# Kernel optimization log

Hardware: AMD Instinct MI355X
Metric: run time of the kernel (lower is better)

The kernel has to match this reference:

```python
import jax, jax.numpy as jnp
import numpy as np

H = 1024      # hidden_dim == memory_dim (required by seq-axis concat)
M = 1024      # memory_dim
FF = 4096     # ff_dim
WIN = 16      # window_size
SLOTS = 10    # persistent memory slots
B, S = 2, 4096
EPS_LN = 1e-5
EPS_NORM = 1e-12


def _layernorm(x, g, b):
    m = jnp.mean(x, axis=-1, keepdims=True)
    v = jnp.var(x, axis=-1, keepdims=True)
    return (x - m) / jnp.sqrt(v + EPS_LN) * g + b


def setup_inputs() -> dict:
    key = jax.random.key(0)
    ks = jax.random.split(key, 12)

    def lin_w(k, out_d, in_d):
        return jax.random.normal(k, (out_d, in_d), jnp.float32) / np.sqrt(in_d)

    return {
        "x": jax.random.normal(ks[0], (B, S, H), jnp.float32),
        "mem_W": lin_w(ks[1], M, M), "mem_b": jnp.zeros((M,), jnp.float32),
        "P": jax.random.normal(ks[2], (SLOTS, M), jnp.float32),
        "Wi": lin_w(ks[3], M, H), "bi": jnp.zeros((M,), jnp.float32),
        "Wl1": lin_w(ks[4], M, M), "bl1": jnp.zeros((M,), jnp.float32),
        "Wl2": lin_w(ks[5], M, M), "bl2": jnp.zeros((M,), jnp.float32),
        "Wo": lin_w(ks[6], H, M), "bo": jnp.zeros((H,), jnp.float32),
        "fgate": jnp.ones((1,), jnp.float32),
        "lrate": jnp.ones((1,), jnp.float32),
        "Wg": lin_w(ks[7], H, 2 * H), "bg": jnp.zeros((H,), jnp.float32),
        "W1": lin_w(ks[8], FF, H), "b1": jnp.zeros((FF,), jnp.float32),
        "W2": lin_w(ks[9], H, FF), "b2": jnp.zeros((H,), jnp.float32),
        "g1": jnp.ones((H,), jnp.float32), "be1": jnp.zeros((H,), jnp.float32),
        "g2": jnp.ones((H,), jnp.float32), "be2": jnp.zeros((H,), jnp.float32),
        "g3": jnp.ones((H,), jnp.float32), "be3": jnp.zeros((H,), jnp.float32),
    }


def reference(x, mem_W, mem_b, P, Wi, bi, Wl1, bl1, Wl2, bl2, Wo, bo,
              fgate, lrate, Wg, bg, W1, b1, W2, b2,
              g1, be1, g2, be2, g3, be3):
    b, s, h = x.shape
    # k = concat(x, persistent) along seq; v = k.clone()
    k_full = jnp.concatenate([x, jnp.broadcast_to(P, (b,) + P.shape)], axis=1)  # [B, S+SLOTS, H]

    # sit at positions >= S and are never inside the window, so only x is attended.
    idx = jnp.arange(s)[:, None] + jnp.arange(-WIN, 1)[None, :]
    valid = idx >= 0
    k_win = k_full[:, jnp.maximum(idx, 0)]
    scores = jnp.einsum('bsh,bswh->bsw', x, k_win) * (h ** -0.5)
    scores = jnp.where(valid[None], scores, -jnp.inf)
    attn_out = jnp.einsum('bsw,bswh->bsh', jax.nn.softmax(scores, axis=-1), k_win)
    x1 = _layernorm(x + attn_out, g1, be1)

    # --- neural long-term memory (key == value since v = k.clone())
    kv = k_full.reshape(-1, h)
    kn = kv / jnp.maximum(jnp.linalg.norm(kv, axis=-1, keepdims=True), EPS_NORM)
    kp = kn @ Wi.T + bi          # projected key; value_proj is identical
    vp = kp
    hdd = jax.nn.silu(kp @ Wl1.T + bl1)
    hdd = jax.nn.silu(hdd @ Wl2.T + bl2)
    pred = hdd @ mem_W.T + mem_b
    diff = pred - vp
    n, m = diff.shape
    grad_W = (2.0 / (n * m)) * diff.T @ hdd          # d mse / d mem_W
    W_new = (1.0 - fgate) * mem_W + lrate * grad_W   # test-time memory update
    mem_out = hdd @ W_new.T + mem_b
    mo = (mem_out @ Wo.T + bo).reshape(b, -1, h)[:, :s]  # align with x seq length

    # --- gated fusion + FFN
    gate = jax.nn.sigmoid(jnp.concatenate([x1, mo], axis=-1) @ Wg.T + bg)
    combined = gate * x1 + (1.0 - gate) * mo
    x2 = _layernorm(x1 + combined, g2, be2)
    ff = jax.nn.silu(x2 @ W1.T + b1) @ W2.T + b2
    return _layernorm(x2 + ff, g3, be3)
```

## Files before the change

kernel.cpp:

```cpp
#include <hip/hip_runtime.h>
#include <hip/hip_bf16.h>

#define WIN 16
#define SLOTS 10
#define SS 4096
#define NTOK 8192
#define NKV 8212
#define NPOS 4106

typedef unsigned short u16;
typedef unsigned int u32;
typedef __attribute__((ext_vector_type(8))) short short8;
typedef __attribute__((ext_vector_type(4))) float f32x4;

__device__ __forceinline__ u16 f2bf(float f){
  union { float f; u32 u; } a; a.f = f;
  u32 r = (a.u + 0x7fff + ((a.u >> 16) & 1)) >> 16;
  return (u16)r;
}
__device__ __forceinline__ float bf2f(u16 v){
  union { u32 u; float f; } a; a.u = ((u32)v) << 16;
  return a.f;
}

#define GLOAD(gp, lp) __builtin_amdgcn_global_load_lds( \
    (const __attribute__((address_space(1))) void*)(gp), \
    (__attribute__((address_space(3))) void*)(lp), 16, 0, 0)

#define FENCE_BARRIER() do { \
    __builtin_amdgcn_sched_barrier(0); \
    __builtin_amdgcn_s_barrier(); \
    __builtin_amdgcn_sched_barrier(0); \
  } while(0)

__global__ __launch_bounds__(256) void cvt_bf16(const float4* __restrict__ in,
                                                ushort4* __restrict__ out, int n4){
  int i = blockIdx.x * 256 + threadIdx.x;
  if (i < n4){
    float4 v = in[i];
    ushort4 o; o.x=f2bf(v.x); o.y=f2bf(v.y); o.z=f2bf(v.z); o.w=f2bf(v.w);
    out[i] = o;
  }
}

__global__ __launch_bounds__(256) void attn_ln1(
    const float* __restrict__ x, const float* __restrict__ g1,
    const float* __restrict__ be1, u16* __restrict__ x1b)
{
  const int n = blockIdx.x;
  const int b = n >> 12, s = n & 4095;
  const int t = threadIdx.x, lane = t & 63, w = t >> 6;
  const float* xb = x + ((size_t)b << 22);
  const float4 q = ((const float4*)(xb + ((size_t)s << 10)))[t];
  const int j0 = (s >= WIN) ? 0 : (WIN - s);
  float kvv[17][4];
  float part[17];
  #pragma unroll
  for (int j=0;j<17;j++){
    float4 kk = make_float4(0.f,0.f,0.f,0.f);
    if (j >= j0) kk = ((const float4*)(xb + ((size_t)(s - WIN + j) << 10)))[t];
    kvv[j][0]=kk.x; kvv[j][1]=kk.y; kvv[j][2]=kk.z; kvv[j][3]=kk.w;
    part[j] = q.x*kk.x + q.y*kk.y + q.z*kk.z + q.w*kk.w;
  }
  __shared__ float red[17][4];
  #pragma unroll
  for (int j=0;j<17;j++){
    float v = part[j];
    #pragma unroll
    for (int off=32; off; off>>=1) v += __shfl_xor(v, off, 64);
    if (lane == 0) red[j][w] = v;
  }
  __syncthreads();
  __shared__ float wsh[17];
  if (t == 0){
    float sc[17];
    float mx = -3.0e38f;
    #pragma unroll
    for (int j=0;j<17;j++){
      float v = (red[j][0]+red[j][1]+red[j][2]+red[j][3]) * 0.03125f;
      sc[j] = v;
      if (j >= j0) mx = fmaxf(mx, v);
    }
    float ssum = 0.f;
    #pragma unroll
    for (int j=0;j<17;j++){
      float e = (j >= j0) ? expf(sc[j]-mx) : 0.f;
      wsh[j] = e; ssum += e;
    }
    float inv = 1.f/ssum;
    #pragma unroll
    for (int j=0;j<17;j++) wsh[j] *= inv;
  }
  __syncthreads();
  float y0=q.x, y1=q.y, y2=q.z, y3=q.w;
  #pragma unroll
  for (int j=0;j<17;j++){
    float wj = wsh[j];
    y0 += wj*kvv[j][0]; y1 += wj*kvv[j][1]; y2 += wj*kvv[j][2]; y3 += wj*kvv[j][3];
  }
  float s1 = y0+y1+y2+y3;
  float s2 = y0*y0+y1*y1+y2*y2+y3*y3;
  #pragma unroll
  for (int off=32; off; off>>=1){ s1 += __shfl_xor(s1, off, 64); s2 += __shfl_xor(s2, off, 64); }
  __shared__ float rsh[8];
  if (lane == 0){ rsh[w] = s1; rsh[4+w] = s2; }
  __syncthreads();
  float S1 = rsh[0]+rsh[1]+rsh[2]+rsh[3];
  float S2 = rsh[4]+rsh[5]+rsh[6]+rsh[7];
  float mean = S1 * (1.f/1024.f);
  float var  = S2 * (1.f/1024.f) - mean*mean;
  float rstd = 1.f/sqrtf(var + 1e-5f);
  float4 gv = ((const float4*)g1)[t];
  float4 bv = ((const float4*)be1)[t];
  ushort4 ob;
  ob.x = f2bf((y0-mean)*rstd*gv.x + bv.x);
  ob.y = f2bf((y1-mean)*rstd*gv.y + bv.y);
  ob.z = f2bf((y2-mean)*rstd*gv.z + bv.z);
  ob.w = f2bf((y3-mean)*rstd*gv.w + bv.w);
  ((ushort4*)x1b)[((size_t)n << 8) + t] = ob;
}

__global__ __launch_bounds__(256) void kv_norm(const float* __restrict__ x,
                                               const float* __restrict__ P,
                                               u16* __restrict__ kn)
{
  const int r = blockIdx.x;
  const int t = threadIdx.x, lane = t & 63, w = t >> 6;
  const int b = r / NPOS;
  const int pos = r - b*NPOS;
  const float* src = (pos < SS) ? (x + (((size_t)b*SS + pos) << 10))
                                : (P + ((size_t)(pos - SS) << 10));
  float4 v = ((const float4*)src)[t];
  float s2 = v.x*v.x + v.y*v.y + v.z*v.z + v.w*v.w;
  #pragma unroll
  for (int off=32; off; off>>=1) s2 += __shfl_xor(s2, off, 64);
  __shared__ float sh[4];
  if (lane == 0) sh[w] = s2;
  __syncthreads();
  float S = sh[0]+sh[1]+sh[2]+sh[3];
  float inv = 1.f / fmaxf(sqrtf(S), 1e-12f);
  ushort4 o; o.x=f2bf(v.x*inv); o.y=f2bf(v.y*inv); o.z=f2bf(v.z*inv); o.w=f2bf(v.w*inv);
  ((ushort4*)kn)[((size_t)r << 8) + t] = o;
}

template<int EPI, int SPLITA>
__global__ __launch_bounds__(256) void gemm_nt(
    const u16* __restrict__ A, const u16* __restrict__ A2,
    const u16* __restrict__ Bmat, const float* __restrict__ bias,
    const u16* __restrict__ auxb,
    float* __restrict__ Cf, u16* __restrict__ Cb,
    int N, int O, int ldA, int ldB, int klen)
{
  __shared__ __align__(16) u16 lA[2][128*64];
  __shared__ __align__(16) u16 lB[2][128*64];
  const int t = threadIdx.x;
  const int lane = t & 63;
  const int bm0 = blockIdx.x * 128;
  const int bn0 = blockIdx.y * 128;
  const int wid = t >> 6;
  const int wr = wid >> 1, wc = wid & 1;
  const int nkt = klen >> 6;

  f32x4 acc[4][4];
  #pragma unroll
  for (int i=0;i<4;i++)
    #pragma unroll
    for (int j=0;j<4;j++)
      acc[i][j] = (f32x4){0.f,0.f,0.f,0.f};

  const int srow = t >> 3;
  const int schunk = (((t & 7) ^ ((t >> 3) & 7)) << 3);

  auto stage = [&](int kt, int buf){
    const int kbase = kt << 6;
    #pragma unroll
    for (int i=0;i<4;i++){
      int gr = bm0 + srow + i*32; gr = gr < N ? gr : N-1;
      const u16* src;
      if (SPLITA){
        src = (kbase < 1024) ? (A  + (size_t)gr*(size_t)ldA + kbase + schunk)
                             : (A2 + ((size_t)gr << 10) + (kbase - 1024) + schunk);
      } else {
        src = A + (size_t)gr*(size_t)ldA + kbase + schunk;
      }
      GLOAD(src, &lA[buf][(i*256 + t) << 3]);
    }
    #pragma unroll
    for (int i=0;i<4;i++){
      int gr = bn0 + srow + i*32; gr = gr < O ? gr : O-1;
      const u16* src = Bmat + (size_t)gr*(size_t)ldB + kbase + schunk;
      GLOAD(src, &lB[buf][(i*256 + t) << 3]);
    }
  };

  stage(0, 0);
  if (nkt > 1) stage(1, 1);

  const int l15 = lane & 15;
  const int rx = l15 & 7;
  const int cq = lane >> 4;

  for (int kt = 0; kt < nkt; ++kt){
    const int cur = kt & 1;
    if (kt + 1 < nkt) { asm volatile("s_waitcnt vmcnt(8)" ::: "memory"); }
    else              { asm volatile("s_waitcnt vmcnt(0)" ::: "memory"); }
    FENCE_BARRIER();
    #pragma unroll
    for (int kk=0;kk<2;kk++){
      const int soff = (((kk*4 + cq) ^ rx) << 3);
      short8 af[4], bfv[4];
      #pragma unroll
      for (int mi=0;mi<4;mi++)
        af[mi] = *(const short8*)(&lA[cur][((wr*64 + mi*16 + l15) << 6) + soff]);
      #pragma unroll
      for (int ni=0;ni<4;ni++)
        bfv[ni] = *(const short8*)(&lB[cur][((wc*64 + ni*16 + l15) << 6) + soff]);
      #pragma unroll
      for (int mi=0;mi<4;mi++)
        #pragma unroll
        for (int ni=0;ni<4;ni++)
          acc[mi][ni] = __builtin_amdgcn_mfma_f32_16x16x32_bf16(af[mi], bfv[ni], acc[mi][ni], 0, 0, 0);
    }
    FENCE_BARRIER();
    if (kt + 2 < nkt) stage(kt + 2, cur);
  }

  const int rbase = (lane >> 4) * 4;
  const int cidx = lane & 15;
  #pragma unroll
  for (int mi=0;mi<4;mi++){
    #pragma unroll
    for (int r=0;r<4;r++){
      const int n = bm0 + wr*64 + mi*16 + rbase + r;
      if (n >= N) continue;
      #pragma unroll
      for (int ni=0;ni<4;ni++){
        const int o = bn0 + wc*64 + ni*16 + cidx;
        float v = acc[mi][ni][r] + bias[o];
        if (EPI == 6){
          int b = n / NPOS;
          int pos = n - b*NPOS;
          if (pos < SS){
            Cb[(((size_t)(b*SS + pos)) << 10) + o] = f2bf(v);
          }
        } else {
          size_t idx = (size_t)n*(size_t)O + o;
          if (EPI == 0){ Cf[idx] = v; }
          else if (EPI == 1){ float sv = v/(1.f+__expf(-v)); Cb[idx] = f2bf(sv); }
          else if (EPI == 2){ Cb[idx] = f2bf(v); }
          else if (EPI == 4){ Cb[idx] = f2bf(v - bf2f(auxb[idx])); }
          else if (EPI == 5){ Cb[idx] = f2bf(1.f/(1.f+__expf(-v))); }
        }
      }
    }
  }
}

#define NSPLIT 6
__global__ __launch_bounds__(256) void gemm_tn(
    const u16* __restrict__ A, const u16* __restrict__ B,
    float* __restrict__ part0, float* __restrict__ part1)
{
  __shared__ __align__(16) u16 lA[128*64];
  __shared__ __align__(16) u16 lB[128*64];
  const int t = threadIdx.x, lane = t & 63;
  const int i0 = blockIdx.x * 128, j0 = blockIdx.y * 128, z = blockIdx.z;
  const int wid = t >> 6, wr = wid >> 1, wc = wid & 1;
  const int TILES = (NKV + 63) >> 6;
  const int PER = (TILES + NSPLIT - 1) / NSPLIT;
  const int kt0 = z * PER;
  const int ktend = (kt0 + PER < TILES) ? (kt0 + PER) : TILES;

  f32x4 acc[4][4];
  #pragma unroll
  for (int i=0;i<4;i++)
    #pragma unroll
    for (int j=0;j<4;j++)
      acc[i][j] = (f32x4){0.f,0.f,0.f,0.f};

  const int p = t & 31;
  const int g = t >> 5;

  auto loadr = [&](int kt, short8 R[8]){
    const int n0 = kt << 6;
    const int na = n0 + 2*p, nb = na + 1;
    short8 z8 = (short8){0,0,0,0,0,0,0,0};
    R[0]=z8;R[1]=z8;R[2]=z8;R[3]=z8;R[4]=z8;R[5]=z8;R[6]=z8;R[7]=z8;
    if (na < NKV){
      const u16* ra = A + (size_t)na*1024 + i0 + g*16;
      R[0] = *(const short8*)ra; R[1] = *(const short8*)(ra+8);
      const u16* rb = B + (size_t)na*1024 + j0 + g*16;
      R[4] = *(const short8*)rb; R[5] = *(const short8*)(rb+8);
    }
    if (nb < NKV){
      const u16* ra = A + (size_t)nb*1024 + i0 + g*16;
      R[2] = *(const short8*)ra; R[3] = *(const short8*)(ra+8);
      const u16* rb = B + (size_t)nb*1024 + j0 + g*16;
      R[6] = *(const short8*)rb; R[7] = *(const short8*)(rb+8);
    }
  };

  short8 cr[8], nr[8];
  loadr(kt0, cr);

  const int pc = p >> 2, pl = p & 3;

  for (int kt = kt0; kt < ktend; ++kt){
    if (kt + 1 < ktend) loadr(kt + 1, nr);
    asm volatile("" ::: "memory");
    FENCE_BARRIER();
    u32* wA = (u32*)lA; u32* wB = (u32*)lB;
    #pragma unroll
    for (int e=0;e<8;e++){
      const int s = (pc ^ e) * 4 + pl;
      wA[(g*16 + e)*32 + s]     = ((u32)(u16)cr[0][e]) | (((u32)(u16)cr[2][e]) << 16);
      wB[(g*16 + e)*32 + s]     = ((u32)(u16)cr[4][e]) | (((u32)(u16)cr[6][e]) << 16);
    }
    #pragma unroll
    for (int e=0;e<8;e++){
      const int s = (pc ^ e) * 4 + pl;
      wA[(g*16 + 8 + e)*32 + s] = ((u32)(u16)cr[1][e]) | (((u32)(u16)cr[3][e]) << 16);
      wB[(g*16 + 8 + e)*32 + s] = ((u32)(u16)cr[5][e]) | (((u32)(u16)cr[7][e]) << 16);
    }
    asm volatile("s_waitcnt lgkmcnt(0)" ::: "memory");
    FENCE_BARRIER();
    const int l15 = lane & 15;
    const int rx = l15 & 7;
    const int cq = lane >> 4;
    #pragma unroll
    for (int kk=0;kk<2;kk++){
      const int soff = (((kk*4 + cq) ^ rx) << 3);
      short8 af[4], bfv[4];
      #pragma unroll
      for (int mi=0;mi<4;mi++)
        af[mi] = *(const short8*)(lA + ((wr*64 + mi*16 + l15) << 6) + soff);
      #pragma unroll
      for (int ni=0;ni<4;ni++)
        bfv[ni] = *(const short8*)(lB + ((wc*64 + ni*16 + l15) << 6) + soff);
      #pragma unroll
      for (int mi=0;mi<4;mi++)
        #pragma unroll
        for (int ni=0;ni<4;ni++)
          acc[mi][ni] = __builtin_amdgcn_mfma_f32_16x16x32_bf16(af[mi], bfv[ni], acc[mi][ni], 0, 0, 0);
    }
    #pragma unroll
    for (int e=0;e<8;e++) cr[e] = nr[e];
  }

  float* dst = (z < 4) ? (part0 + ((size_t)z << 20)) : (part1 + ((size_t)(z-4) << 20));
  const int rbase = (lane >> 4) * 4;
  const int cidx = lane & 15;
  #pragma unroll
  for (int mi=0;mi<4;mi++)
    #pragma unroll
    for (int r=0;r<4;r++){
      const int i = i0 + wr*64 + mi*16 + rbase + r;
      #pragma unroll
      for (int ni=0;ni<4;ni++){
        const int j = j0 + wc*64 + ni*16 + cidx;
        dst[((size_t)i << 10) + j] = acc[mi][ni][r];
      }
    }
}

__global__ __launch_bounds__(256) void wnew_k(const float* __restrict__ part0,
                                              const float* __restrict__ part1,
                                              const float* __restrict__ memW,
                                              const float* __restrict__ fg,
                                              const float* __restrict__ lr,
                                              u16* __restrict__ out)
{
  int i = blockIdx.x*256 + threadIdx.x;
  float s = part0[i] + part0[i + (1<<20)] + part0[i + (2<<20)] + part0[i + (3<<20)]
          + part1[i] + part1[i + (1<<20)];
  const float scale = 2.f / ((float)NKV * 1024.f);
  float v = (1.f - fg[0])*memW[i] + lr[0]*scale*s;
  out[i] = f2bf(v);
}

__global__ __launch_bounds__(256) void ln_gate(
    const u16* __restrict__ x1b, const u16* __restrict__ gateb,
    const u16* __restrict__ mob, const float* __restrict__ g2,
    const float* __restrict__ be2, u16* __restrict__ x2b)
{
  const int n = blockIdx.x;
  const int t = threadIdx.x, lane = t & 63, w = t >> 6;
  const size_t rb = (size_t)n << 8;
  ushort4 xa = ((const ushort4*)x1b)[rb+t];
  ushort4 ga = ((const ushort4*)gateb)[rb+t];
  ushort4 ma = ((const ushort4*)mob)[rb+t];
  float a0=bf2f(xa.x),a1=bf2f(xa.y),a2=bf2f(xa.z),a3=bf2f(xa.w);
  float g0=bf2f(ga.x),g1v=bf2f(ga.y),g2v=bf2f(ga.z),g3v=bf2f(ga.w);
  float m0=bf2f(ma.x),m1=bf2f(ma.y),m2=bf2f(ma.z),m3=bf2f(ma.w);
  float y0 = a0 + g0*a0 + (1.f-g0)*m0;
  float y1 = a1 + g1v*a1 + (1.f-g1v)*m1;
  float y2 = a2 + g2v*a2 + (1.f-g2v)*m2;
  float y3 = a3 + g3v*a3 + (1.f-g3v)*m3;
  float s1 = y0+y1+y2+y3;
  float s2 = y0*y0+y1*y1+y2*y2+y3*y3;
  #pragma unroll
  for (int off=32; off; off>>=1){ s1 += __shfl_xor(s1, off, 64); s2 += __shfl_xor(s2, off, 64); }
  __shared__ float rsh[8];
  if (lane == 0){ rsh[w] = s1; rsh[4+w] = s2; }
  __syncthreads();
  float S1 = rsh[0]+rsh[1]+rsh[2]+rsh[3];
  float S2 = rsh[4]+rsh[5]+rsh[6]+rsh[7];
  float mean = S1 * (1.f/1024.f);
  float var  = S2 * (1.f/1024.f) - mean*mean;
  float rstd = 1.f/sqrtf(var + 1e-5f);
  float4 gv = ((const float4*)g2)[t];
  float4 bv = ((const float4*)be2)[t];
  ushort4 ob;
  ob.x = f2bf((y0-mean)*rstd*gv.x + bv.x);
  ob.y = f2bf((y1-mean)*rstd*gv.y + bv.y);
  ob.z = f2bf((y2-mean)*rstd*gv.z + bv.z);
  ob.w = f2bf((y3-mean)*rstd*gv.w + bv.w);
  ((ushort4*)x2b)[rb + t] = ob;
}

__global__ __launch_bounds__(256) void ln_final(
    const u16* __restrict__ x2b, const float* __restrict__ g3,
    const float* __restrict__ be3, float* __restrict__ out)
{
  const int n = blockIdx.x;
  const int t = threadIdx.x, lane = t & 63, w = t >> 6;
  const size_t rb = (size_t)n << 8;
  ushort4 xa = ((const ushort4*)x2b)[rb+t];
  float4 f = ((const float4*)out)[rb+t];
  float y0 = bf2f(xa.x)+f.x, y1 = bf2f(xa.y)+f.y, y2 = bf2f(xa.z)+f.z, y3 = bf2f(xa.w)+f.w;
  float s1 = y0+y1+y2+y3;
  float s2 = y0*y0+y1*y1+y2*y2+y3*y3;
  #pragma unroll
  for (int off=32; off; off>>=1){ s1 += __shfl_xor(s1, off, 64); s2 += __shfl_xor(s2, off, 64); }
  __shared__ float rsh[8];
  if (lane == 0){ rsh[w] = s1; rsh[4+w] = s2; }
  __syncthreads();
  float S1 = rsh[0]+rsh[1]+rsh[2]+rsh[3];
  float S2 = rsh[4]+rsh[5]+rsh[6]+rsh[7];
  float mean = S1 * (1.f/1024.f);
  float var  = S2 * (1.f/1024.f) - mean*mean;
  float rstd = 1.f/sqrtf(var + 1e-5f);
  float4 gv = ((const float4*)g3)[t];
  float4 bv = ((const float4*)be3)[t];
  float4 o;
  o.x = (y0-mean)*rstd*gv.x + bv.x;
  o.y = (y1-mean)*rstd*gv.y + bv.y;
  o.z = (y2-mean)*rstd*gv.z + bv.z;
  o.w = (y3-mean)*rstd*gv.w + bv.w;
  ((float4*)out)[rb + t] = o;
}

extern "C" void kernel_launch(void* const* d_in, const int* in_sizes, int n_in,
                              void* d_out, int out_size, void* d_ws, size_t ws_size,
                              hipStream_t stream)
{
  const float* x    = (const float*)d_in[0];
  const float* memW = (const float*)d_in[1];
  const float* memb = (const float*)d_in[2];
  const float* P    = (const float*)d_in[3];
  const float* Wi   = (const float*)d_in[4];
  const float* bi   = (const float*)d_in[5];
  const float* Wl1  = (const float*)d_in[6];
  const float* bl1  = (const float*)d_in[7];
  const float* Wl2  = (const float*)d_in[8];
  const float* bl2  = (const float*)d_in[9];
  const float* Wo   = (const float*)d_in[10];
  const float* bo   = (const float*)d_in[11];
  const float* fg   = (const float*)d_in[12];
  const float* lr   = (const float*)d_in[13];
  const float* Wg   = (const float*)d_in[14];
  const float* bg   = (const float*)d_in[15];
  const float* W1   = (const float*)d_in[16];
  const float* b1   = (const float*)d_in[17];
  const float* W2   = (const float*)d_in[18];
  const float* b2   = (const float*)d_in[19];
  const float* g1   = (const float*)d_in[20];
  const float* be1  = (const float*)d_in[21];
  const float* g2   = (const float*)d_in[22];
  const float* be2  = (const float*)d_in[23];
  const float* g3   = (const float*)d_in[24];
  const float* be3  = (const float*)d_in[25];
  float* out = (float*)d_out;

  const size_t SZ_TOK = (size_t)NTOK*1024*2;
  const size_t SZ_KV  = (size_t)NKV*1024*2;
  char* base = (char*)d_ws;
  size_t off = 0;
  auto alloc = [&](size_t bytes) -> char* {
    char* p = base + off;
    off += (bytes + 255) & ~(size_t)255;
    return p;
  };
  u16* x1b   = (u16*)alloc(SZ_TOK);
  u16* knb   = (u16*)alloc(SZ_KV);
  u16* h1b   = (u16*)alloc(SZ_KV);
  u16* hddb  = (u16*)alloc(SZ_KV);
  u16* kpb   = (u16*)alloc(SZ_KV);
  u16* wnewb = (u16*)alloc((size_t)1024*1024*2);
  u16* WiB   = (u16*)alloc((size_t)1024*1024*2);
  u16* Wl1B  = (u16*)alloc((size_t)1024*1024*2);
  u16* Wl2B  = (u16*)alloc((size_t)1024*1024*2);
  u16* memWB = (u16*)alloc((size_t)1024*1024*2);
  u16* WoB   = (u16*)alloc((size_t)1024*1024*2);
  u16* WgB   = (u16*)alloc((size_t)1024*2048*2);
  u16* W1B   = (u16*)alloc((size_t)4096*1024*2);
  u16* W2B   = (u16*)alloc((size_t)1024*4096*2);
  if (ws_size < off) return;

  u16*   diffb   = knb;
  float* part0   = (float*)kpb;
  float* part1   = (float*)WiB;
  u16*   memoutb = knb;
  u16*   mob     = h1b;
  u16*   gateb   = hddb;
  u16*   x2b     = kpb;
  u16*   ff1b    = x1b;

  auto cvt = [&](const float* src, u16* dst, int nelem){
    cvt_bf16<<<nelem/1024, 256, 0, stream>>>((const float4*)src, (ushort4*)dst, nelem/4);
  };
  cvt(Wi,   WiB,   1024*1024);
  cvt(Wl1,  Wl1B,  1024*1024);
  cvt(Wl2,  Wl2B,  1024*1024);
  cvt(memW, memWB, 1024*1024);
  cvt(Wo,   WoB,   1024*1024);
  cvt(Wg,   WgB,   1024*2048);
  cvt(W1,   W1B,   4096*1024);
  cvt(W2,   W2B,   1024*4096);

  attn_ln1<<<NTOK, 256, 0, stream>>>(x, g1, be1, x1b);
  kv_norm <<<NKV,  256, 0, stream>>>(x, P, knb);

  dim3 gkv(65, 8, 1);
  gemm_nt<2,0><<<gkv, 256, 0, stream>>>(knb, nullptr, WiB, bi, nullptr, nullptr, kpb, NKV, 1024, 1024, 1024, 1024);
  gemm_nt<1,0><<<gkv, 256, 0, stream>>>(kpb, nullptr, Wl1B, bl1, nullptr, nullptr, h1b, NKV, 1024, 1024, 1024, 1024);
  gemm_nt<1,0><<<gkv, 256, 0, stream>>>(h1b, nullptr, Wl2B, bl2, nullptr, nullptr, hddb, NKV, 1024, 1024, 1024, 1024);
  gemm_nt<4,0><<<gkv, 256, 0, stream>>>(hddb, nullptr, memWB, memb, kpb, nullptr, diffb, NKV, 1024, 1024, 1024, 1024);
  gemm_tn<<<dim3(8, 8, NSPLIT), 256, 0, stream>>>(diffb, hddb, part0, part1);
  wnew_k<<<4096, 256, 0, stream>>>(part0, part1, memW, fg, lr, wnewb);
  gemm_nt<2,0><<<gkv, 256, 0, stream>>>(hddb, nullptr, wnewb, memb, nullptr, nullptr, memoutb, NKV, 1024, 1024, 1024, 1024);
  gemm_nt<6,0><<<gkv, 256, 0, stream>>>(memoutb, nullptr, WoB, bo, nullptr, nullptr, mob, NKV, 1024, 1024, 1024, 1024);
  gemm_nt<5,1><<<dim3(64, 8, 1), 256, 0, stream>>>(x1b, mob, WgB, bg, nullptr, nullptr, gateb, NTOK, 1024, 1024, 2048, 2048);
  ln_gate<<<NTOK, 256, 0, stream>>>(x1b, gateb, mob, g2, be2, x2b);
  gemm_nt<1,0><<<dim3(64, 32, 1), 256, 0, stream>>>(x2b, nullptr, W1B, b1, nullptr, nullptr, ff1b, NTOK, 4096, 1024, 1024, 1024);
  gemm_nt<0,0><<<dim3(64, 8, 1), 256, 0, stream>>>(ff1b, nullptr, W2B, b2, nullptr, out, nullptr, NTOK, 1024, 4096, 4096, 4096);
  ln_final<<<NTOK, 256, 0, stream>>>(x2b, g3, be3, out);
}
```

Baseline: 654.7 us.

## Add 256x256-tile GEMM kernel for FFN up-projection and hoist load address math

Result: no change. 649.6 us (-0.8%).

```diff
diff --git a/kernel.cpp b/kernel.cpp
--- a/kernel.cpp
+++ b/kernel.cpp
@@ -169,28 +169,29 @@
       acc[i][j] = (f32x4){0.f,0.f,0.f,0.f};
 
   const int srow = t >> 3;
-  const int schunk = (((t & 7) ^ ((t >> 3) & 7)) << 3);
+  const int schunk = (((t & 7) ^ (srow & 7)) << 3);
+
+  const u16* baseA[4]; const u16* baseA2[4]; const u16* baseB[4];
+  #pragma unroll
+  for (int i=0;i<4;i++){
+    int gr = bm0 + srow + i*32; gr = gr < N ? gr : N-1;
+    baseA[i] = A + (size_t)gr*(size_t)ldA + schunk;
+    if (SPLITA) baseA2[i] = A2 + ((size_t)gr << 10) + schunk;
+    int gb = bn0 + srow + i*32; gb = gb < O ? gb : O-1;
+    baseB[i] = Bmat + (size_t)gb*(size_t)ldB + schunk;
+  }
 
   auto stage = [&](int kt, int buf){
-    const int kbase = kt << 6;
+    const int kb = kt << 6;
     #pragma unroll
     for (int i=0;i<4;i++){
-      int gr = bm0 + srow + i*32; gr = gr < N ? gr : N-1;
-      const u16* src;
-      if (SPLITA){
-        src = (kbase < 1024) ? (A  + (size_t)gr*(size_t)ldA + kbase + schunk)
-                             : (A2 + ((size_t)gr << 10) + (kbase - 1024) + schunk);
-      } else {
-        src = A + (size_t)gr*(size_t)ldA + kbase + schunk;
-      }
+      const u16* src = SPLITA ? ((kb < 1024) ? baseA[i] + kb : baseA2[i] + (kb - 1024))
+                              : baseA[i] + kb;
       GLOAD(src, &lA[buf][(i*256 + t) << 3]);
     }
     #pragma unroll
-    for (int i=0;i<4;i++){
-      int gr = bn0 + srow + i*32; gr = gr < O ? gr : O-1;
-      const u16* src = Bmat + (size_t)gr*(size_t)ldB + kbase + schunk;
-      GLOAD(src, &lB[buf][(i*256 + t) << 3]);
-    }
+    for (int i=0;i<4;i++)
+      GLOAD(baseB[i] + kb, &lB[buf][(i*256 + t) << 3]);
   };
 
   stage(0, 0);
@@ -251,6 +252,105 @@
           else if (EPI == 4){ Cb[idx] = f2bf(v - bf2f(auxb[idx])); }
           else if (EPI == 5){ Cb[idx] = f2bf(1.f/(1.f+__expf(-v))); }
         }
+      }
+    }
+  }
+}
+
+template<int EPI>
+__global__ __launch_bounds__(512, 2) void gemm_256(
+    const u16* __restrict__ A, const u16* __restrict__ Bmat,
+    const float* __restrict__ bias,
+    float* __restrict__ Cf, u16* __restrict__ Cb,
+    int N, int O, int ldA, int ldB, int klen)
+{
+  __shared__ __align__(16) u16 lA[2][256*64];
+  __shared__ __align__(16) u16 lB[2][256*64];
+  const int t = threadIdx.x;
+  const int lane = t & 63;
+  const int wid = t >> 6;
+  const int wr = wid >> 2, wc = wid & 3;
+  const int bm0 = blockIdx.x * 256;
+  const int bn0 = blockIdx.y * 256;
+  const int nkt = klen >> 6;
+
+  f32x4 acc[8][4];
+  #pragma unroll
+  for (int i=0;i<8;i++)
+    #pragma unroll
+    for (int j=0;j<4;j++)
+      acc[i][j] = (f32x4){0.f,0.f,0.f,0.f};
+
+  const int srow = t >> 3;
+  const int schunk = (((t & 7) ^ (srow & 7)) << 3);
+
+  const u16* baseA[4]; const u16* baseB[4];
+  #pragma unroll
+  for (int i=0;i<4;i++){
+    int gr = bm0 + srow + i*64; gr = gr < N ? gr : N-1;
+    baseA[i] = A + (size_t)gr*(size_t)ldA + schunk;
+    int gb = bn0 + srow + i*64; gb = gb < O ? gb : O-1;
+    baseB[i] = Bmat + (size_t)gb*(size_t)ldB + schunk;
+  }
+
+  auto stage = [&](int kt, int buf){
+    const int kb = kt << 6;
+    #pragma unroll
+    for (int i=0;i<4;i++)
+      GLOAD(baseA[i] + kb, &lA[buf][(i*512 + t) << 3]);
+    #pragma unroll
+    for (int i=0;i<4;i++)
+      GLOAD(baseB[i] + kb, &lB[buf][(i*512 + t) << 3]);
+  };
+
+  stage(0, 0);
+  if (nkt > 1) stage(1, 1);
+
+  const int l15 = lane & 15;
+  const int rx = l15 & 7;
+  const int cq = lane >> 4;
+
+  for (int kt = 0; kt < nkt; ++kt){
+    const int cur = kt & 1;
+    if (kt + 1 < nkt) { asm volatile("s_waitcnt vmcnt(8)" ::: "memory"); }
+    else              { asm volatile("s_waitcnt vmcnt(0)" ::: "memory"); }
+    FENCE_BARRIER();
+    #pragma unroll
+    for (int kk=0;kk<2;kk++){
+      const int soff = (((kk*4 + cq) ^ rx) << 3);
+      short8 af[8], bfv[4];
+      #pragma unroll
+      for (int ni=0;ni<4;ni++)
+        bfv[ni] = *(const short8*)(&lB[cur][((wc*64 + ni*16 + l15) << 6) + soff]);
+      #pragma unroll
+      for (int mi=0;mi<8;mi++)
+        af[mi] = *(const short8*)(&lA[cur][((wr*128 + mi*16 + l15) << 6) + soff]);
+      #pragma unroll
+      for (int mi=0;mi<8;mi++)
+        #pragma unroll
+        for (int ni=0;ni<4;ni++)
+          acc[mi][ni] = __builtin_amdgcn_mfma_f32_16x16x32_bf16(af[mi], bfv[ni], acc[mi][ni], 0, 0, 0);
+    }
+    FENCE_BARRIER();
+    if (kt + 2 < nkt) stage(kt + 2, cur);
+  }
+
+  const int rbase = (lane >> 4) * 4;
+  const int cidx = lane & 15;
+  #pragma unroll
+  for (int mi=0;mi<8;mi++){
+    #pragma unroll
+    for (int r=0;r<4;r++){
+      const int n = bm0 + wr*128 + mi*16 + rbase + r;
+      if (n >= N) continue;
+      #pragma unroll
+      for (int ni=0;ni<4;ni++){
+        const int o = bn0 + wc*64 + ni*16 + cidx;
+        float v = acc[mi][ni][r] + bias[o];
+        size_t idx = (size_t)n*(size_t)O + o;
+        if (EPI == 0){ Cf[idx] = v; }
+        else if (EPI == 1){ float sv = v/(1.f+__expf(-v)); Cb[idx] = f2bf(sv); }
+        else if (EPI == 2){ Cb[idx] = f2bf(v); }
       }
     }
   }
@@ -542,7 +642,7 @@
   gemm_nt<6,0><<<gkv, 256, 0, stream>>>(memoutb, nullptr, WoB, bo, nullptr, nullptr, mob, NKV, 1024, 1024, 1024, 1024);
   gemm_nt<5,1><<<dim3(64, 8, 1), 256, 0, stream>>>(x1b, mob, WgB, bg, nullptr, nullptr, gateb, NTOK, 1024, 1024, 2048, 2048);
   ln_gate<<<NTOK, 256, 0, stream>>>(x1b, gateb, mob, g2, be2, x2b);
-  gemm_nt<1,0><<<dim3(64, 32, 1), 256, 0, stream>>>(x2b, nullptr, W1B, b1, nullptr, nullptr, ff1b, NTOK, 4096, 1024, 1024, 1024);
+  gemm_256<1><<<dim3(32, 16, 1), 512, 0, stream>>>(x2b, W1B, b1, nullptr, ff1b, NTOK, 4096, 1024, 1024, 1024);
   gemm_nt<0,0><<<dim3(64, 8, 1), 256, 0, stream>>>(ff1b, nullptr, W2B, b2, nullptr, out, nullptr, NTOK, 1024, 4096, 4096, 4096);
   ln_final<<<NTOK, 256, 0, stream>>>(x2b, g3, be3, out);
 }
```
